# Performance work log

Hardware: AMD Instinct MI355X
Metric: run time of the kernel (lower is better)

## Reference

```python
import jax, jax.numpy as jnp
import numpy as np

CUTOFF = 5.0
LOG2 = 0.6931471805599453

def ssp(x):
    # ShiftedSoftplus: softplus(x) - log(2)
    return jax.nn.softplus(x) - LOG2

def setup_inputs() -> dict:
    key = jax.random.key(0)
    ks = jax.random.split(key, 10)
    B, P, A, G, F, E = 2, 4096, 96, 1, 32, 20
    return {
        "scalar": jax.random.normal(ks[0], (B, A, G, F), jnp.float32),
        "scalar_reciever": jax.random.normal(ks[1], (B, P, G, F), jnp.float32),
        "expansion": jax.random.uniform(ks[2], (B, P, A, E), jnp.float32),
        "mask": jax.random.uniform(ks[3], (B, P, A, G), jnp.float32),
        "edge_distance": jax.random.uniform(ks[4], (B, P, A, 1), jnp.float32) * CUTOFF,
        "W1e": jax.random.normal(ks[5], (E, F), jnp.float32) * 0.1,
        "b1e": jnp.zeros((F,), jnp.float32),
        "W2e": jax.random.normal(ks[6], (F, F), jnp.float32) * 0.1,
        "b2e": jnp.zeros((F,), jnp.float32),
        "W1n": jax.random.normal(ks[7], (2 * F, F), jnp.float32) * 0.1,
        "b1n": jnp.zeros((F,), jnp.float32),
        "W2n": jax.random.normal(ks[8], (F, F), jnp.float32) * 0.1,
        "b2n": jnp.zeros((F,), jnp.float32),
    }

def reference(scalar, scalar_reciever, expansion, mask, edge_distance,
              W1e, b1e, W2e, b2e, W1n, b1n, W2n, b2n):
    F = scalar.shape[-1]
    # edge gate: 2-layer MLP on expansion, times soft cutoff  -> [B,P,A,F]
    gates = ssp(expansion @ W1e + b1e) @ W2e + b2e
    gates = gates * (1.0 - jax.nn.sigmoid(5.0 * (edge_distance - (CUTOFF - 1.5))))
    # pairwise node MLP: split first linear into source/target halves instead of
    # materializing the [B,P,A,G,2F] repeat+concat tensor (same math).
    Ws, Wt = W1n[:F], W1n[F:]
    src = jnp.einsum('bagf,fh->bagh', scalar, Ws)            # [B,A,G,H]
    tgt = jnp.einsum('bpgf,fh->bpgh', scalar_reciever, Wt)   # [B,P,G,H]
    h = src[:, None, :, :, :] + tgt[:, :, None, :, :] + b1n  # [B,P,A,G,H]
    nodes = ssp(h) @ W2n + b2n                               # [B,P,A,G,F]
    result = mask[..., None] * (gates[..., None, :] * nodes)
    return jnp.sum(result, axis=-3)                          # sum over atoms A -> [B,P,G,F]

if __name__ == "__main__":
    out = reference(**setup_inputs())
    print(out.shape)
```

## Files before the change

kernel.cpp:

```cpp
#include <hip/hip_runtime.h>

#define NB   2
#define NP   4096
#define NA   96
#define NF   32
#define NE   20
#define NBP  (NB*NP)

typedef __attribute__((ext_vector_type(8)))  short bf16x8;
typedef __attribute__((ext_vector_type(16))) float f32x16;

union Frag { bf16x8 v; int i[4]; };

__device__ __forceinline__ int cvtpk(float lo, float hi) {
  int r;
  asm("v_cvt_pk_bf16_f32 %0, %1, %2" : "=v"(r) : "v"(lo), "v"(hi));
  return r;
}
__device__ __forceinline__ float ssp_f(float x) {
  float t = __expf(-fabsf(x));
  return fmaxf(x, 0.0f) + __logf(1.0f + t) - 0.69314718056f;
}
__device__ __forceinline__ f32x16 mfma32(const Frag a, const Frag b, f32x16 c) {
  return __builtin_amdgcn_mfma_f32_32x32x16_bf16(a.v, b.v, c, 0, 0, 0);
}
__device__ __forceinline__ f32x16 ld_bias16(const float* __restrict__ base ) {
  const float4* p = reinterpret_cast<const float4*>(base);
  float4 q0 = p[0], q1 = p[2], q2 = p[4], q3 = p[6];
  f32x16 c;
  c[0]=q0.x;  c[1]=q0.y;  c[2]=q0.z;  c[3]=q0.w;
  c[4]=q1.x;  c[5]=q1.y;  c[6]=q1.z;  c[7]=q1.w;
  c[8]=q2.x;  c[9]=q2.y;  c[10]=q2.z; c[11]=q2.w;
  c[12]=q3.x; c[13]=q3.y; c[14]=q3.z; c[15]=q3.w;
  return c;
}

__global__ __launch_bounds__(256)
void prep_src(const float* __restrict__ scalar,
              const float* __restrict__ W1n,
              const float* __restrict__ b1n,
              float* __restrict__ src_ws)
{
  int i = blockIdx.x * 256 + threadIdx.x;
  int f  = i & 31;
  int ba = i >> 5;
  const float* x = scalar + ba * NF;
  float a = b1n[f];
#pragma unroll
  for (int k = 0; k < NF; ++k) a = fmaf(x[k], W1n[k * NF + f], a);
  src_ws[i] = a;
}

__global__ __launch_bounds__(256, 3)
void fused_main(const float* __restrict__ expansion,
                const float* __restrict__ mask,
                const float* __restrict__ edge_dist,
                const float* __restrict__ W1e,
                const float* __restrict__ b1e,
                const float* __restrict__ W2e,
                const float* __restrict__ b2e,
                const float* __restrict__ W2n,
                const float* __restrict__ b2n,
                const float* __restrict__ sr,
                const float* __restrict__ W1n,
                const float* __restrict__ src_ws,
                float* __restrict__ out)
{
  const int tid  = threadIdx.x;
  const int wid  = tid >> 6;
  const int lane = tid & 63;
  const int col  = lane & 31;
  const int hw   = lane >> 5;

  Frag a1s0, a1s1, a2s0, a2s1, a3s0, a3s1;
#pragma unroll
  for (int r = 0; r < 4; ++r) {
    const int k0 = 8 * hw + 2 * r;
    const int k1 = 16 + k0;
    a1s0.i[r] = cvtpk(W1e[k0 * NF + col], W1e[(k0 + 1) * NF + col]);
    {
      float lo = (k1     < NE) ? W1e[k1 * NF + col]       : 0.0f;
      float hi = (k1 + 1 < NE) ? W1e[(k1 + 1) * NF + col] : 0.0f;
      a1s1.i[r] = cvtpk(lo, hi);
    }
    a2s0.i[r] = cvtpk(W2e[k0 * NF + col], W2e[(k0 + 1) * NF + col]);
    a2s1.i[r] = cvtpk(W2e[k1 * NF + col], W2e[(k1 + 1) * NF + col]);
    a3s0.i[r] = cvtpk(W2n[k0 * NF + col], W2n[(k0 + 1) * NF + col]);
    a3s1.i[r] = cvtpk(W2n[k1 * NF + col], W2n[(k1 + 1) * NF + col]);
  }

  float wt[16];
#pragma unroll
  for (int i2 = 0; i2 < 16; ++i2) wt[i2] = W1n[(NF + 16 * hw + i2) * NF + col];

#pragma unroll 1
  for (int pi = 0; pi < 2; ++pi) {
    const int bp = blockIdx.x * 8 + wid * 2 + pi;
    const int b  = bp >> 12;

    const float* srow = sr + bp * NF + 16 * hw;
    float ts = 0.0f;
#pragma unroll
    for (int i2 = 0; i2 < 16; ++i2) ts = fmaf(srow[i2], wt[i2], ts);
    ts += __shfl_xor(ts, 32, 64);
    float tA[8], tB[8];
#pragma unroll
    for (int j = 0; j < 8; ++j) {
      tA[j] = __shfl(ts,      8 * hw + j, 64);
      tB[j] = __shfl(ts, 16 + 8 * hw + j, 64);
    }

    const float* expb  = expansion + (size_t)bp * (NA * NE);
    const float* maskb = mask      + bp * NA;
    const float* distb = edge_dist + bp * NA;
    const float* srcb  = src_ws    + b * (NA * NF);

    f32x16 acc;
#pragma unroll
    for (int r = 0; r < 16; ++r) acc[r] = 0.0f;

#pragma unroll 1
    for (int t = 0; t < 3; ++t) {
      const int a = t * 32 + col;

      const float* ea = expb + a * NE;
      float4 e0 = *reinterpret_cast<const float4*>(ea + 8 * hw);
      float4 e1 = *reinterpret_cast<const float4*>(ea + 8 * hw + 4);
      float4 e2 = *reinterpret_cast<const float4*>(ea + 16);
      Frag b1f0, b1f1;
      b1f0.i[0] = cvtpk(e0.x, e0.y);
      b1f0.i[1] = cvtpk(e0.z, e0.w);
      b1f0.i[2] = cvtpk(e1.x, e1.y);
      b1f0.i[3] = cvtpk(e1.z, e1.w);
      b1f1.i[0] = hw ? 0 : cvtpk(e2.x, e2.y);
      b1f1.i[1] = hw ? 0 : cvtpk(e2.z, e2.w);
      b1f1.i[2] = 0;
      b1f1.i[3] = 0;

      f32x16 d1 = ld_bias16(b1e + 4 * hw);
      d1 = mfma32(a1s0, b1f0, d1);
      d1 = mfma32(a1s1, b1f1, d1);
#pragma unroll
      for (int r = 0; r < 16; ++r) d1[r] = ssp_f(d1[r]);

      int u0 = cvtpk(d1[0],  d1[1]);
      int u1 = cvtpk(d1[2],  d1[3]);
      int u2 = cvtpk(d1[4],  d1[5]);
      int u3 = cvtpk(d1[6],  d1[7]);
      int u4 = cvtpk(d1[8],  d1[9]);
      int u5 = cvtpk(d1[10], d1[11]);
      int u6 = cvtpk(d1[12], d1[13]);
      int u7 = cvtpk(d1[14], d1[15]);
      asm("v_permlane32_swap_b32 %0, %1" : "+v"(u0), "+v"(u2));
      asm("v_permlane32_swap_b32 %0, %1" : "+v"(u1), "+v"(u3));
      asm("v_permlane32_swap_b32 %0, %1" : "+v"(u4), "+v"(u6));
      asm("v_permlane32_swap_b32 %0, %1" : "+v"(u5), "+v"(u7));
      Frag b2f0, b2f1;
      b2f0.i[0] = u0; b2f0.i[1] = u1; b2f0.i[2] = u2; b2f0.i[3] = u3;
      b2f1.i[0] = u4; b2f1.i[1] = u5; b2f1.i[2] = u6; b2f1.i[3] = u7;

      f32x16 d2 = ld_bias16(b2e + 4 * hw);
      d2 = mfma32(a2s0, b2f0, d2);
      d2 = mfma32(a2s1, b2f1, d2);

      const float mk = maskb[a];
      const float dd = distb[a];
      const float z  = __expf(5.0f * (dd - 3.5f));
      const float em = mk * __builtin_amdgcn_rcpf(1.0f + z);

      const float* sa = srcb + a * NF;
      float4 s0 = *reinterpret_cast<const float4*>(sa + 8 * hw);
      float4 s1 = *reinterpret_cast<const float4*>(sa + 8 * hw + 4);
      float4 s2 = *reinterpret_cast<const float4*>(sa + 16 + 8 * hw);
      float4 s3 = *reinterpret_cast<const float4*>(sa + 16 + 8 * hw + 4);
      Frag b3f0, b3f1;
      b3f0.i[0] = cvtpk(ssp_f(s0.x + tA[0]), ssp_f(s0.y + tA[1]));
      b3f0.i[1] = cvtpk(ssp_f(s0.z + tA[2]), ssp_f(s0.w + tA[3]));
      b3f0.i[2] = cvtpk(ssp_f(s1.x + tA[4]), ssp_f(s1.y + tA[5]));
      b3f0.i[3] = cvtpk(ssp_f(s1.z + tA[6]), ssp_f(s1.w + tA[7]));
      b3f1.i[0] = cvtpk(ssp_f(s2.x + tB[0]), ssp_f(s2.y + tB[1]));
      b3f1.i[1] = cvtpk(ssp_f(s2.z + tB[2]), ssp_f(s2.w + tB[3]));
      b3f1.i[2] = cvtpk(ssp_f(s3.x + tB[4]), ssp_f(s3.y + tB[5]));
      b3f1.i[3] = cvtpk(ssp_f(s3.z + tB[6]), ssp_f(s3.w + tB[7]));

      f32x16 d3 = ld_bias16(b2n + 4 * hw);
      d3 = mfma32(a3s0, b3f0, d3);
      d3 = mfma32(a3s1, b3f1, d3);

#pragma unroll
      for (int r = 0; r < 16; ++r) acc[r] = fmaf(em * d2[r], d3[r], acc[r]);
    }

#pragma unroll
    for (int m = 1; m <= 16; m <<= 1) {
#pragma unroll
      for (int r = 0; r < 16; ++r) acc[r] += __shfl_xor(acc[r], m, 64);
    }

    if (col == 0) {
      float4* o = reinterpret_cast<float4*>(out + bp * NF);
#pragma unroll
      for (int q = 0; q < 4; ++q) {
        float4 v;
        v.x = acc[4 * q];     v.y = acc[4 * q + 1];
        v.z = acc[4 * q + 2]; v.w = acc[4 * q + 3];
        o[2 * q + hw] = v;
      }
    }
  }
}

extern "C" void kernel_launch(void* const* d_in, const int* in_sizes, int n_in,
                              void* d_out, int out_size, void* d_ws, size_t ws_size,
                              hipStream_t stream) {
  const float* scalar    = (const float*)d_in[0];
  const float* sreciever = (const float*)d_in[1];
  const float* expansion = (const float*)d_in[2];
  const float* maskp     = (const float*)d_in[3];
  const float* edist     = (const float*)d_in[4];
  const float* W1e       = (const float*)d_in[5];
  const float* b1e       = (const float*)d_in[6];
  const float* W2e       = (const float*)d_in[7];
  const float* b2e       = (const float*)d_in[8];
  const float* W1n       = (const float*)d_in[9];
  const float* b1n       = (const float*)d_in[10];
  const float* W2n       = (const float*)d_in[11];
  const float* b2n       = (const float*)d_in[12];
  float* out    = (float*)d_out;
  float* src_ws = (float*)d_ws;

  prep_src<<<24, 256, 0, stream>>>(scalar, W1n, b1n, src_ws);
  fused_main<<<NBP / 8, 256, 0, stream>>>(expansion, maskp, edist,
                                          W1e, b1e, W2e, b2e, W2n, b2n,
                                          sreciever, W1n, src_ws, out);
}
```

Measured before the change: 167.1 us.

## Precompute target projection in prep kernel, prefetch atom inputs, stage biases in LDS

The receiver-side linear projection moves out of the main kernel into the prep kernel and is staged in the output buffer, which the main kernel reads back before overwriting it. This removes the per-wave dot product and shuffle broadcast. The main kernel now loads all expansion, mask and distance values for the three atom tiles up front and fully unrolls the atom loop so loads can overlap compute. Biases are staged in shared memory. The cost is higher register pressure and a larger prep launch, and reusing the output buffer as scratch depends on each wave reading its row before writing it.

```diff
diff --git a/kernel.cpp b/kernel.cpp
--- a/kernel.cpp
+++ b/kernel.cpp
@@ -24,7 +24,7 @@
 __device__ __forceinline__ f32x16 mfma32(const Frag a, const Frag b, f32x16 c) {
   return __builtin_amdgcn_mfma_f32_32x32x16_bf16(a.v, b.v, c, 0, 0, 0);
 }
-__device__ __forceinline__ f32x16 ld_bias16(const float* __restrict__ base ) {
+__device__ __forceinline__ f32x16 ld_bias16(const float* base ) {
   const float4* p = reinterpret_cast<const float4*>(base);
   float4 q0 = p[0], q1 = p[2], q2 = p[4], q3 = p[6];
   f32x16 c;
@@ -36,19 +36,33 @@
 }
 
 __global__ __launch_bounds__(256)
-void prep_src(const float* __restrict__ scalar,
-              const float* __restrict__ W1n,
-              const float* __restrict__ b1n,
-              float* __restrict__ src_ws)
+void prep_kernel(const float* __restrict__ scalar,
+                 const float* __restrict__ sr,
+                 const float* __restrict__ W1n,
+                 const float* __restrict__ b1n,
+                 float* __restrict__ tgt_out,
+                 float* __restrict__ src_ws)
 {
   int i = blockIdx.x * 256 + threadIdx.x;
-  int f  = i & 31;
-  int ba = i >> 5;
-  const float* x = scalar + ba * NF;
-  float a = b1n[f];
-#pragma unroll
-  for (int k = 0; k < NF; ++k) a = fmaf(x[k], W1n[k * NF + f], a);
-  src_ws[i] = a;
+  int f   = i & 31;
+  int row = i >> 5;
+  const float* x;
+  const float* W;
+  float acc;
+  if (row < NBP) { x = sr + row * NF;            W = W1n + NF * NF; acc = 0.0f;   }
+  else           { x = scalar + (row - NBP) * NF; W = W1n;          acc = b1n[f]; }
+  float4 xv[8];
+#pragma unroll
+  for (int q = 0; q < 8; ++q) xv[q] = reinterpret_cast<const float4*>(x)[q];
+#pragma unroll
+  for (int q = 0; q < 8; ++q) {
+    acc = fmaf(xv[q].x, W[(4 * q + 0) * NF + f], acc);
+    acc = fmaf(xv[q].y, W[(4 * q + 1) * NF + f], acc);
+    acc = fmaf(xv[q].z, W[(4 * q + 2) * NF + f], acc);
+    acc = fmaf(xv[q].w, W[(4 * q + 3) * NF + f], acc);
+  }
+  if (row < NBP) tgt_out[i] = acc;
+  else           src_ws[(row - NBP) * NF + f] = acc;
 }
 
 __global__ __launch_bounds__(256, 3)
@@ -61,8 +75,6 @@
                 const float* __restrict__ b2e,
                 const float* __restrict__ W2n,
                 const float* __restrict__ b2n,
-                const float* __restrict__ sr,
-                const float* __restrict__ W1n,
                 const float* __restrict__ src_ws,
                 float* __restrict__ out)
 {
@@ -72,6 +84,17 @@
   const int col  = lane & 31;
   const int hw   = lane >> 5;
 
+  __shared__ __align__(16) float smb[96];
+  if (tid < 32) {
+    smb[tid]      = b1e[tid];
+    smb[32 + tid] = b2e[tid];
+    smb[64 + tid] = b2n[tid];
+  }
+  __syncthreads();
+  const float* biasA = smb      + 4 * hw;
+  const float* biasB = smb + 32 + 4 * hw;
+  const float* biasC = smb + 64 + 4 * hw;
+
   Frag a1s0, a1s1, a2s0, a2s1, a3s0, a3s1;
 #pragma unroll
   for (int r = 0; r < 4; ++r) {
@@ -89,55 +112,60 @@
     a3s1.i[r] = cvtpk(W2n[k1 * NF + col], W2n[(k1 + 1) * NF + col]);
   }
 
-  float wt[16];
-#pragma unroll
-  for (int i2 = 0; i2 < 16; ++i2) wt[i2] = W1n[(NF + 16 * hw + i2) * NF + col];
-
 #pragma unroll 1
   for (int pi = 0; pi < 2; ++pi) {
     const int bp = blockIdx.x * 8 + wid * 2 + pi;
     const int b  = bp >> 12;
 
-    const float* srow = sr + bp * NF + 16 * hw;
-    float ts = 0.0f;
-#pragma unroll
-    for (int i2 = 0; i2 < 16; ++i2) ts = fmaf(srow[i2], wt[i2], ts);
-    ts += __shfl_xor(ts, 32, 64);
-    float tA[8], tB[8];
-#pragma unroll
-    for (int j = 0; j < 8; ++j) {
-      tA[j] = __shfl(ts,      8 * hw + j, 64);
-      tB[j] = __shfl(ts, 16 + 8 * hw + j, 64);
-    }
+    const float* tg = out + bp * NF;
+    float4 t0 = *reinterpret_cast<const float4*>(tg + 8 * hw);
+    float4 t1 = *reinterpret_cast<const float4*>(tg + 8 * hw + 4);
+    float4 t2 = *reinterpret_cast<const float4*>(tg + 16 + 8 * hw);
+    float4 t3 = *reinterpret_cast<const float4*>(tg + 16 + 8 * hw + 4);
 
     const float* expb  = expansion + (size_t)bp * (NA * NE);
     const float* maskb = mask      + bp * NA;
     const float* distb = edge_dist + bp * NA;
     const float* srcb  = src_ws    + b * (NA * NF);
 
-    f32x16 acc;
-#pragma unroll
-    for (int r = 0; r < 16; ++r) acc[r] = 0.0f;
-
-#pragma unroll 1
+    float4 ef[3][3];
+    float  mk[3], dd[3];
+#pragma unroll
     for (int t = 0; t < 3; ++t) {
       const int a = t * 32 + col;
-
       const float* ea = expb + a * NE;
-      float4 e0 = *reinterpret_cast<const float4*>(ea + 8 * hw);
-      float4 e1 = *reinterpret_cast<const float4*>(ea + 8 * hw + 4);
-      float4 e2 = *reinterpret_cast<const float4*>(ea + 16);
+      ef[t][0] = *reinterpret_cast<const float4*>(ea + 8 * hw);
+      ef[t][1] = *reinterpret_cast<const float4*>(ea + 8 * hw + 4);
+      ef[t][2] = *reinterpret_cast<const float4*>(ea + 16);
+      mk[t] = maskb[a];
+      dd[t] = distb[a];
+    }
+    float em[3];
+#pragma unroll
+    for (int t = 0; t < 3; ++t) {
+      const float z = __expf(5.0f * (dd[t] - 3.5f));
+      em[t] = mk[t] * __builtin_amdgcn_rcpf(1.0f + z);
+    }
+
+    f32x16 acc;
+#pragma unroll
+    for (int r = 0; r < 16; ++r) acc[r] = 0.0f;
+
+#pragma unroll
+    for (int t = 0; t < 3; ++t) {
+      const int a = t * 32 + col;
+
       Frag b1f0, b1f1;
-      b1f0.i[0] = cvtpk(e0.x, e0.y);
-      b1f0.i[1] = cvtpk(e0.z, e0.w);
-      b1f0.i[2] = cvtpk(e1.x, e1.y);
-      b1f0.i[3] = cvtpk(e1.z, e1.w);
-      b1f1.i[0] = hw ? 0 : cvtpk(e2.x, e2.y);
-      b1f1.i[1] = hw ? 0 : cvtpk(e2.z, e2.w);
+      b1f0.i[0] = cvtpk(ef[t][0].x, ef[t][0].y);
+      b1f0.i[1] = cvtpk(ef[t][0].z, ef[t][0].w);
+      b1f0.i[2] = cvtpk(ef[t][1].x, ef[t][1].y);
+      b1f0.i[3] = cvtpk(ef[t][1].z, ef[t][1].w);
+      b1f1.i[0] = hw ? 0 : cvtpk(ef[t][2].x, ef[t][2].y);
+      b1f1.i[1] = hw ? 0 : cvtpk(ef[t][2].z, ef[t][2].w);
       b1f1.i[2] = 0;
       b1f1.i[3] = 0;
 
-      f32x16 d1 = ld_bias16(b1e + 4 * hw);
+      f32x16 d1 = ld_bias16(biasA);
       d1 = mfma32(a1s0, b1f0, d1);
       d1 = mfma32(a1s1, b1f1, d1);
 #pragma unroll
@@ -159,14 +187,9 @@
       b2f0.i[0] = u0; b2f0.i[1] = u1; b2f0.i[2] = u2; b2f0.i[3] = u3;
       b2f1.i[0] = u4; b2f1.i[1] = u5; b2f1.i[2] = u6; b2f1.i[3] = u7;
 
-      f32x16 d2 = ld_bias16(b2e + 4 * hw);
+      f32x16 d2 = ld_bias16(biasB);
       d2 = mfma32(a2s0, b2f0, d2);
       d2 = mfma32(a2s1, b2f1, d2);
-
-      const float mk = maskb[a];
-      const float dd = distb[a];
-      const float z  = __expf(5.0f * (dd - 3.5f));
-      const float em = mk * __builtin_amdgcn_rcpf(1.0f + z);
 
       const float* sa = srcb + a * NF;
       float4 s0 = *reinterpret_cast<const float4*>(sa + 8 * hw);
@@ -174,21 +197,21 @@
       float4 s2 = *reinterpret_cast<const float4*>(sa + 16 + 8 * hw);
       float4 s3 = *reinterpret_cast<const float4*>(sa + 16 + 8 * hw + 4);
       Frag b3f0, b3f1;
-      b3f0.i[0] = cvtpk(ssp_f(s0.x + tA[0]), ssp_f(s0.y + tA[1]));
-      b3f0.i[1] = cvtpk(ssp_f(s0.z + tA[2]), ssp_f(s0.w + tA[3]));
-      b3f0.i[2] = cvtpk(ssp_f(s1.x + tA[4]), ssp_f(s1.y + tA[5]));
-      b3f0.i[3] = cvtpk(ssp_f(s1.z + tA[6]), ssp_f(s1.w + tA[7]));
-      b3f1.i[0] = cvtpk(ssp_f(s2.x + tB[0]), ssp_f(s2.y + tB[1]));
-      b3f1.i[1] = cvtpk(ssp_f(s2.z + tB[2]), ssp_f(s2.w + tB[3]));
-      b3f1.i[2] = cvtpk(ssp_f(s3.x + tB[4]), ssp_f(s3.y + tB[5]));
-      b3f1.i[3] = cvtpk(ssp_f(s3.z + tB[6]), ssp_f(s3.w + tB[7]));
-
-      f32x16 d3 = ld_bias16(b2n + 4 * hw);
+      b3f0.i[0] = cvtpk(ssp_f(s0.x + t0.x), ssp_f(s0.y + t0.y));
+      b3f0.i[1] = cvtpk(ssp_f(s0.z + t0.z), ssp_f(s0.w + t0.w));
+      b3f0.i[2] = cvtpk(ssp_f(s1.x + t1.x), ssp_f(s1.y + t1.y));
+      b3f0.i[3] = cvtpk(ssp_f(s1.z + t1.z), ssp_f(s1.w + t1.w));
+      b3f1.i[0] = cvtpk(ssp_f(s2.x + t2.x), ssp_f(s2.y + t2.y));
+      b3f1.i[1] = cvtpk(ssp_f(s2.z + t2.z), ssp_f(s2.w + t2.w));
+      b3f1.i[2] = cvtpk(ssp_f(s3.x + t3.x), ssp_f(s3.y + t3.y));
+      b3f1.i[3] = cvtpk(ssp_f(s3.z + t3.z), ssp_f(s3.w + t3.w));
+
+      f32x16 d3 = ld_bias16(biasC);
       d3 = mfma32(a3s0, b3f0, d3);
       d3 = mfma32(a3s1, b3f1, d3);
 
 #pragma unroll
-      for (int r = 0; r < 16; ++r) acc[r] = fmaf(em * d2[r], d3[r], acc[r]);
+      for (int r = 0; r < 16; ++r) acc[r] = fmaf(em[t] * d2[r], d3[r], acc[r]);
     }
 
 #pragma unroll
@@ -229,8 +252,8 @@
   float* out    = (float*)d_out;
   float* src_ws = (float*)d_ws;
 
-  prep_src<<<24, 256, 0, stream>>>(scalar, W1n, b1n, src_ws);
+  prep_kernel<<<1048, 256, 0, stream>>>(scalar, sreciever, W1n, b1n, out, src_ws);
   fused_main<<<NBP / 8, 256, 0, stream>>>(expansion, maskp, edist,
                                           W1e, b1e, W2e, b2e, W2n, b2n,
-                                          sreciever, W1n, src_ws, out);
-}
+                                          src_ws, out);
+}
```

New measurement: 149.8 us. 10.4% less time.
